# Kernel optimization log

Hardware: AMD Instinct MI355X
Metric: run time of the kernel (lower is better)

The kernel has to match this reference:

```python
import jax, jax.numpy as jnp
import numpy as np

B, H, S, DK = 2, 16, 2048, 64
NEG = -1000000000.0

def setup_inputs() -> dict:
    key = jax.random.key(0)
    k1, k2, k3, k4 = jax.random.split(key, 4)
    Q = jax.random.normal(k1, (B, H, S, DK), dtype=jnp.float32)
    K = jax.random.normal(k2, (B, H, S, DK), dtype=jnp.float32)
    V = jax.random.normal(k3, (B, H, S, DK), dtype=jnp.float32)
    mask = jax.random.randint(k4, (B, 1, S, S), 0, 2).astype(bool)
    return {"Q": Q, "K": K, "V": V, "mask": mask}

def reference(Q, K, V, mask):
    sqrt_dk = jnp.asarray(DK ** 0.5, Q.dtype)
    # [B,H,S,S] scores, materialized as in the original module
    score = jnp.einsum('bhqd,bhkd->bhqk', Q, K) / sqrt_dk
    score = jnp.where(mask, jnp.asarray(NEG, score.dtype), score)
    attn_prob = jax.nn.softmax(score, axis=-1)  # dropout p=0.0 -> identity
    context = jnp.einsum('bhqk,bhkd->bhqd', attn_prob, V)
    return (context, attn_prob)
```

## Files before the change

### kernel.cpp

```cpp
#include <hip/hip_runtime.h>

static constexpr int Bc  = 2;
static constexpr int Hc  = 16;
static constexpr int Sc  = 2048;
static constexpr int DKc = 64;
static constexpr float SC2  = 0.18033688011112043f;

typedef __attribute__((ext_vector_type(8)))  short short8v;
typedef __attribute__((ext_vector_type(16))) float f32x16;
typedef __attribute__((ext_vector_type(4)))  float f32x4;

__device__ __forceinline__ unsigned short f2bf(float f) {
    union { float f; unsigned u; } v; v.f = f;
    unsigned r = v.u + 0x7FFFu + ((v.u >> 16) & 1u);
    return (unsigned short)(r >> 16);
}
__device__ __forceinline__ unsigned cvtpk(float lo, float hi) {
    unsigned r;
    asm("v_cvt_pk_bf16_f32 %0, %1, %2" : "=v"(r) : "v"(lo), "v"(hi));
    return r;
}
__device__ __forceinline__ float fexp2(float x) {
    float r;
    asm("v_exp_f32 %0, %1" : "=v"(r) : "v"(x));
    return r;
}
__device__ __forceinline__ float bflo(unsigned u) {
    union { unsigned u; float f; } v; v.u = u << 16; return v.f;
}
__device__ __forceinline__ float bfhi(unsigned u) {
    union { unsigned u; float f; } v; v.u = u & 0xFFFF0000u; return v.f;
}

__global__ void kfrag_kernel(const float* __restrict__ K, unsigned short* __restrict__ Kf) {
    int i = blockIdx.x * 256 + threadIdx.x;
    int lane = i & 63, ks = (i >> 6) & 3, t = (i >> 8) & 63, bh = i >> 14;
    int hi = lane >> 5, l31 = lane & 31;
    const float* src = K + (((size_t)bh * Sc + t * 32 + l31) * DKc + ks * 16 + hi * 8);
    float4 a = *(const float4*)src;
    float4 c = *(const float4*)(src + 4);
    short8v s;
    s[0]=(short)f2bf(a.x); s[1]=(short)f2bf(a.y); s[2]=(short)f2bf(a.z); s[3]=(short)f2bf(a.w);
    s[4]=(short)f2bf(c.x); s[5]=(short)f2bf(c.y); s[6]=(short)f2bf(c.z); s[7]=(short)f2bf(c.w);
    *(short8v*)&Kf[(size_t)i * 8] = s;
}

__global__ void vfrag_kernel(const float* __restrict__ V, unsigned short* __restrict__ Vf) {
    int i = blockIdx.x * 256 + threadIdx.x;
    int lane = i & 63, dblk = (i >> 6) & 1, ks = (i >> 7) & 1, t = (i >> 8) & 63, bh = i >> 14;
    int hi = lane >> 5, l31 = lane & 31;
    int k0 = t * 32 + ks * 16 + hi * 8, d = dblk * 32 + l31;
    const float* vb = V + ((size_t)bh * Sc + k0) * DKc + d;
    short8v s;
    #pragma unroll
    for (int u = 0; u < 8; ++u) s[u] = (short)f2bf(vb[(size_t)u * DKc]);
    *(short8v*)&Vf[(size_t)i * 8] = s;
}

__global__ void mfrag_kernel(const int* __restrict__ M, unsigned* __restrict__ Mf) {
    int w = blockIdx.x * 4 + (threadIdx.x >> 6);
    int lane = threadIdx.x & 63;
    const int* row = M + (size_t)w * Sc;
    int b = w >> 11, q = w & 2047, qt = q >> 5, r = q & 31;
    unsigned* ob = Mf + (size_t)(b * 64 + qt) * 2048 + r;
    for (int tp = 0; tp < 32; ++tp) {
        unsigned long long bal = __ballot(row[tp * 64 + lane] != 0);
        if (lane == 0)  ob[(size_t)(2 * tp)     * 32] = (unsigned)bal;
        if (lane == 32) ob[(size_t)(2 * tp + 1) * 32] = (unsigned)(bal >> 32);
    }
}

__global__ __launch_bounds__(256, 2)
void attn_main(const float* __restrict__ Q, const unsigned short* __restrict__ Kf,
               const unsigned short* __restrict__ Vf, const unsigned* __restrict__ Mf,
               float* __restrict__ out)
{
    const int wg  = (int)blockIdx.x;
    const int swz = (wg & 7) * 256 + (wg >> 3);
    const int bh  = swz >> 6;
    const int qt  = swz & 63;
    const int qb  = qt << 5;
    const int b   = bh >> 4;

    const int tid  = (int)threadIdx.x;
    const int wid  = tid >> 6;
    const int lane = tid & 63;
    const int hi   = lane >> 5;
    const int l31  = lane & 31;

    __shared__ float lbuf[4][32];
    __shared__ float lfin[32];
    __shared__ char  sbuf[2][32768];

    const unsigned short* kfb = Kf + (size_t)bh * 131072;
    const unsigned short* vfb = Vf + (size_t)bh * 131072;
    const unsigned*       mfb = Mf + (size_t)(b * 64 + qt) * 2048;

    short8v qf[4];
    {
        const float* qrow = Q + ((size_t)bh * Sc + qb + l31) * DKc;
        #pragma unroll
        for (int ks = 0; ks < 4; ++ks) {
            const float* p0 = qrow + ks * 16 + hi * 8;
            float4 a = *(const float4*)p0;
            float4 c = *(const float4*)(p0 + 4);
            short8v f;
            f[0]=(short)f2bf(a.x); f[1]=(short)f2bf(a.y); f[2]=(short)f2bf(a.z); f[3]=(short)f2bf(a.w);
            f[4]=(short)f2bf(c.x); f[5]=(short)f2bf(c.y); f[6]=(short)f2bf(c.z); f[7]=(short)f2bf(c.w);
            qf[ks] = f;
        }
    }

    f32x16 acc0, acc1;
    #pragma unroll
    for (int u = 0; u < 16; ++u) { acc0[u] = 0.0f; acc1[u] = 0.0f; }

    unsigned ec[16][8];
    float l_run = 0.0f;

    #pragma unroll
    for (int i = 0; i < 16; ++i) {
        const int t = i * 4 + wid;
        short8v k4[4];
        #pragma unroll
        for (int ks = 0; ks < 4; ++ks)
            k4[ks] = *(const short8v*)&kfb[((size_t)(t * 4 + ks) * 64 + lane) * 8];
        short8v v4[4];
        #pragma unroll
        for (int u = 0; u < 4; ++u)
            v4[u] = *(const short8v*)&vfb[((size_t)(t * 4 + u) * 64 + lane) * 8];
        const unsigned mw = mfb[t * 32 + l31] >> (4 * hi);

        f32x16 sc;
        #pragma unroll
        for (int u = 0; u < 16; ++u) sc[u] = 0.0f;
        #pragma unroll
        for (int ks = 0; ks < 4; ++ks)
            sc = __builtin_amdgcn_mfma_f32_32x32x16_bf16(k4[ks], qf[ks], sc, 0, 0, 0);

        #pragma unroll
        for (int g = 0; g < 4; ++g)
            #pragma unroll
            for (int j = 0; j < 4; ++j) {
                float a = sc[4*g+j] * SC2;
                a = ((mw >> (8*g + j)) & 1u) ? -1e30f : a;
                sc[4*g+j] = fexp2(a);
            }

        float ps = 0.0f;
        #pragma unroll
        for (int u = 0; u < 16; ++u) ps += sc[u];
        ps += __shfl_xor(ps, 32);
        l_run += ps;

        #pragma unroll
        for (int g = 0; g < 4; ++g) {
            ec[i][2*g]   = cvtpk(sc[4*g],   sc[4*g+1]);
            ec[i][2*g+1] = cvtpk(sc[4*g+2], sc[4*g+3]);
        }

        #pragma unroll
        for (int ks = 0; ks < 2; ++ks) {
            unsigned o0x = ec[i][4*ks], o0y = ec[i][4*ks+1];
            unsigned o1x = ec[i][4*ks+2], o1y = ec[i][4*ks+3];
            unsigned s0x = __shfl_xor(o0x, 32), s0y = __shfl_xor(o0y, 32);
            unsigned s1x = __shfl_xor(o1x, 32), s1y = __shfl_xor(o1y, 32);
            union { unsigned u[4]; short8v s; } pa;
            pa.u[0] = hi ? s1x : o0x;
            pa.u[1] = hi ? s1y : o0y;
            pa.u[2] = hi ? o1x : s0x;
            pa.u[3] = hi ? o1y : s0y;
            acc0 = __builtin_amdgcn_mfma_f32_32x32x16_bf16(pa.s, v4[2*ks+0], acc0, 0, 0, 0);
            acc1 = __builtin_amdgcn_mfma_f32_32x32x16_bf16(pa.s, v4[2*ks+1], acc1, 0, 0, 0);
        }
    }

    if (hi == 0) lbuf[wid][l31] = l_run;
    __syncthreads();
    if (tid < 32) lfin[tid] = lbuf[0][tid] + lbuf[1][tid] + lbuf[2][tid] + lbuf[3][tid];
    __syncthreads();
    const float inv_l = 1.0f / lfin[l31];

    float* ctx   = out;
    float* attn  = out + (size_t)Bc * Hc * Sc * DKc;
    float* prow0 = attn + ((size_t)bh * Sc + qb) * Sc;

    #pragma unroll
    for (int r = 0; r < 8; ++r) {
        char* sb = &sbuf[r & 1][0];
        #pragma unroll
        for (int sub = 0; sub < 2; ++sub) {
            const int i = r * 2 + sub;
            #pragma unroll
            for (int g = 0; g < 4; ++g) {
                unsigned u0 = ec[i][2*g], u1 = ec[i][2*g+1];
                f32x4 st;
                st.x = bflo(u0) * inv_l; st.y = bfhi(u0) * inv_l;
                st.z = bflo(u1) * inv_l; st.w = bfhi(u1) * inv_l;
                *(f32x4*)(sb + sub * 16384 + l31 * 512 +
                          ((wid * 128 + 32*g + 16*hi) ^ ((l31 & 7) << 4))) = st;
            }
        }
        __syncthreads();
        #pragma unroll
        for (int j = 0; j < 8; ++j) {
            const int row = j * 4 + wid;
            f32x4 ld = *(const f32x4*)(&sbuf[r & 1][0] + (lane >> 5) * 16384 + row * 512 +
                                       (((lane & 31) * 16) ^ ((row & 7) << 4)));
            __builtin_nontemporal_store(ld, (f32x4*)(prow0 + (size_t)row * Sc + r * 256 + lane * 4));
        }
    }

    __syncthreads();
    float* pall = (float*)&sbuf[0][0];
    if (wid >= 2) {
        #pragma unroll
        for (int g = 0; g < 4; ++g)
            #pragma unroll
            for (int j = 0; j < 4; ++j) {
                int row = 8*g + 4*hi + j;
                pall[(wid - 2) * 2048 + row * 64 + l31]      = acc0[4*g+j];
                pall[(wid - 2) * 2048 + row * 64 + l31 + 32] = acc1[4*g+j];
            }
    }
    __syncthreads();
    if (wid < 2) {
        #pragma unroll
        for (int g = 0; g < 4; ++g)
            #pragma unroll
            for (int j = 0; j < 4; ++j) {
                int row = 8*g + 4*hi + j;
                acc0[4*g+j] += pall[wid * 2048 + row * 64 + l31];
                acc1[4*g+j] += pall[wid * 2048 + row * 64 + l31 + 32];
            }
    }
    __syncthreads();
    if (wid == 1) {
        #pragma unroll
        for (int g = 0; g < 4; ++g)
            #pragma unroll
            for (int j = 0; j < 4; ++j) {
                int row = 8*g + 4*hi + j;
                pall[row * 64 + l31]      = acc0[4*g+j];
                pall[row * 64 + l31 + 32] = acc1[4*g+j];
            }
    }
    __syncthreads();
    if (wid == 0) {
        #pragma unroll
        for (int g = 0; g < 4; ++g)
            #pragma unroll
            for (int j = 0; j < 4; ++j) {
                int row = 8*g + 4*hi + j;
                float rinv = 1.0f / lfin[row];
                float o0 = (acc0[4*g+j] + pall[row * 64 + l31])      * rinv;
                float o1 = (acc1[4*g+j] + pall[row * 64 + l31 + 32]) * rinv;
                size_t off = ((size_t)bh * Sc + qb + row) * DKc + l31;
                ctx[off]      = o0;
                ctx[off + 32] = o1;
            }
    }
}

extern "C" void kernel_launch(void* const* d_in, const int* in_sizes, int n_in,
                              void* d_out, int out_size, void* d_ws, size_t ws_size,
                              hipStream_t stream)
{
    const float* Q = (const float*)d_in[0];
    const float* K = (const float*)d_in[1];
    const float* V = (const float*)d_in[2];
    const int*   M = (const int*)d_in[3];
    float* out = (float*)d_out;

    unsigned short* Kf = (unsigned short*)d_ws;
    unsigned short* Vf = (unsigned short*)((char*)d_ws + (8u << 20));
    unsigned*       Mf = (unsigned*)((char*)d_ws + (16u << 20));

    hipLaunchKernelGGL(kfrag_kernel, dim3(2048), dim3(256), 0, stream, K, Kf);
    hipLaunchKernelGGL(vfrag_kernel, dim3(2048), dim3(256), 0, stream, V, Vf);
    hipLaunchKernelGGL(mfrag_kernel, dim3(1024), dim3(256), 0, stream, M, Mf);
    hipLaunchKernelGGL(attn_main,    dim3(2048), dim3(256), 0, stream, Q, Kf, Vf, Mf, out);
}
```

Measured before the change: 173.8 us.

## Make attention blocks persistent over four query tiles, overlapping prob stores with compute

Each workgroup now has 8 waves and loops over 4 consecutive query tiles of the same head instead of one. The attention-probability write-back for the previous tile is interleaved into the QK/PV loop of the next tile through a single shared staging buffer, so the heavy global store traffic overlaps with MFMA work. The split-K reduction across waves now has 8 partial accumulators. Costs include extra barriers inside the main loop, fewer workgroups (512), and more register pressure at 512 threads per block.

```diff
diff --git a/kernel.cpp b/kernel.cpp
--- a/kernel.cpp
+++ b/kernel.cpp
@@ -70,16 +70,15 @@
     }
 }
 
-__global__ __launch_bounds__(256, 2)
+__global__ __launch_bounds__(512, 2)
 void attn_main(const float* __restrict__ Q, const unsigned short* __restrict__ Kf,
                const unsigned short* __restrict__ Vf, const unsigned* __restrict__ Mf,
                float* __restrict__ out)
 {
     const int wg  = (int)blockIdx.x;
-    const int swz = (wg & 7) * 256 + (wg >> 3);
-    const int bh  = swz >> 6;
-    const int qt  = swz & 63;
-    const int qb  = qt << 5;
+    const int swz = (wg & 7) * 64 + (wg >> 3);
+    const int bh  = swz >> 4;
+    const int qt0 = (swz & 15) * 4;
     const int b   = bh >> 4;
 
     const int tid  = (int)threadIdx.x;
@@ -88,177 +87,237 @@
     const int hi   = lane >> 5;
     const int l31  = lane & 31;
 
-    __shared__ float lbuf[4][32];
+    __shared__ float lbuf[8][32];
     __shared__ float lfin[32];
-    __shared__ char  sbuf[2][32768];
+    __shared__ char  sbuf[32768];
 
     const unsigned short* kfb = Kf + (size_t)bh * 131072;
     const unsigned short* vfb = Vf + (size_t)bh * 131072;
-    const unsigned*       mfb = Mf + (size_t)(b * 64 + qt) * 2048;
-
-    short8v qf[4];
-    {
-        const float* qrow = Q + ((size_t)bh * Sc + qb + l31) * DKc;
+
+    float* ctx  = out;
+    float* attn = out + (size_t)Bc * Hc * Sc * DKc;
+
+    float  inv_prev  = 0.0f;
+    float* prow_prev = nullptr;
+
+    unsigned ec[8][8];
+
+    for (int tt = 0; tt < 4; ++tt) {
+        const int qt = qt0 + tt;
+        const int qb = qt * 32;
+        const unsigned* mfb = Mf + (size_t)(b * 64 + qt) * 2048;
+
+        short8v qf[4];
+        {
+            const float* qrow = Q + ((size_t)bh * Sc + qb + l31) * DKc;
+            #pragma unroll
+            for (int ks = 0; ks < 4; ++ks) {
+                const float* p0 = qrow + ks * 16 + hi * 8;
+                float4 a = *(const float4*)p0;
+                float4 c = *(const float4*)(p0 + 4);
+                short8v f;
+                f[0]=(short)f2bf(a.x); f[1]=(short)f2bf(a.y); f[2]=(short)f2bf(a.z); f[3]=(short)f2bf(a.w);
+                f[4]=(short)f2bf(c.x); f[5]=(short)f2bf(c.y); f[6]=(short)f2bf(c.z); f[7]=(short)f2bf(c.w);
+                qf[ks] = f;
+            }
+        }
+
+        f32x16 acc0, acc1;
         #pragma unroll
-        for (int ks = 0; ks < 4; ++ks) {
-            const float* p0 = qrow + ks * 16 + hi * 8;
-            float4 a = *(const float4*)p0;
-            float4 c = *(const float4*)(p0 + 4);
-            short8v f;
-            f[0]=(short)f2bf(a.x); f[1]=(short)f2bf(a.y); f[2]=(short)f2bf(a.z); f[3]=(short)f2bf(a.w);
-            f[4]=(short)f2bf(c.x); f[5]=(short)f2bf(c.y); f[6]=(short)f2bf(c.z); f[7]=(short)f2bf(c.w);
-            qf[ks] = f;
-        }
+        for (int u = 0; u < 16; ++u) { acc0[u] = 0.0f; acc1[u] = 0.0f; }
+        float l_run = 0.0f;
+
+        #pragma unroll
+        for (int i = 0; i < 8; ++i) {
+            if (tt > 0) {
+                __syncthreads();
+                #pragma unroll
+                for (int g = 0; g < 4; ++g) {
+                    unsigned u0 = ec[i][2*g], u1 = ec[i][2*g+1];
+                    f32x4 st;
+                    st.x = bflo(u0) * inv_prev; st.y = bfhi(u0) * inv_prev;
+                    st.z = bflo(u1) * inv_prev; st.w = bfhi(u1) * inv_prev;
+                    *(f32x4*)(sbuf + l31 * 1024 + wid * 128 +
+                              ((32*g + 16*hi) ^ ((l31 & 7) << 4))) = st;
+                }
+                __syncthreads();
+            }
+
+            const int t = i * 8 + wid;
+            short8v k4[4];
+            #pragma unroll
+            for (int ks = 0; ks < 4; ++ks)
+                k4[ks] = *(const short8v*)&kfb[((size_t)(t * 4 + ks) * 64 + lane) * 8];
+            short8v v4[4];
+            #pragma unroll
+            for (int u = 0; u < 4; ++u)
+                v4[u] = *(const short8v*)&vfb[((size_t)(t * 4 + u) * 64 + lane) * 8];
+            const unsigned mw = mfb[t * 32 + l31] >> (4 * hi);
+
+            if (tt > 0) {
+                #pragma unroll
+                for (int j = 0; j < 4; ++j) {
+                    const int row = j * 8 + wid;
+                    const int cb = lane * 16;
+                    f32x4 ld = *(const f32x4*)(sbuf + row * 1024 + (cb & ~127) +
+                                               ((cb & 127) ^ ((row & 7) << 4)));
+                    __builtin_nontemporal_store(ld,
+                        (f32x4*)(prow_prev + (size_t)row * Sc + i * 256 + lane * 4));
+                }
+            }
+
+            f32x16 sc;
+            #pragma unroll
+            for (int u = 0; u < 16; ++u) sc[u] = 0.0f;
+            #pragma unroll
+            for (int ks = 0; ks < 4; ++ks)
+                sc = __builtin_amdgcn_mfma_f32_32x32x16_bf16(k4[ks], qf[ks], sc, 0, 0, 0);
+
+            #pragma unroll
+            for (int g = 0; g < 4; ++g)
+                #pragma unroll
+                for (int j = 0; j < 4; ++j) {
+                    float a = sc[4*g+j] * SC2;
+                    a = ((mw >> (8*g + j)) & 1u) ? -1e30f : a;
+                    sc[4*g+j] = fexp2(a);
+                }
+
+            float ps = 0.0f;
+            #pragma unroll
+            for (int u = 0; u < 16; ++u) ps += sc[u];
+            ps += __shfl_xor(ps, 32);
+            l_run += ps;
+
+            #pragma unroll
+            for (int g = 0; g < 4; ++g) {
+                ec[i][2*g]   = cvtpk(sc[4*g],   sc[4*g+1]);
+                ec[i][2*g+1] = cvtpk(sc[4*g+2], sc[4*g+3]);
+            }
+
+            #pragma unroll
+            for (int ks = 0; ks < 2; ++ks) {
+                unsigned o0x = ec[i][4*ks], o0y = ec[i][4*ks+1];
+                unsigned o1x = ec[i][4*ks+2], o1y = ec[i][4*ks+3];
+                unsigned s0x = __shfl_xor(o0x, 32), s0y = __shfl_xor(o0y, 32);
+                unsigned s1x = __shfl_xor(o1x, 32), s1y = __shfl_xor(o1y, 32);
+                union { unsigned u[4]; short8v s; } pa;
+                pa.u[0] = hi ? s1x : o0x;
+                pa.u[1] = hi ? s1y : o0y;
+                pa.u[2] = hi ? o1x : s0x;
+                pa.u[3] = hi ? o1y : s0y;
+                acc0 = __builtin_amdgcn_mfma_f32_32x32x16_bf16(pa.s, v4[2*ks+0], acc0, 0, 0, 0);
+                acc1 = __builtin_amdgcn_mfma_f32_32x32x16_bf16(pa.s, v4[2*ks+1], acc1, 0, 0, 0);
+            }
+        }
+
+        if (hi == 0) lbuf[wid][l31] = l_run;
+        __syncthreads();
+        if (tid < 32) {
+            float l = 0.0f;
+            #pragma unroll
+            for (int w = 0; w < 8; ++w) l += lbuf[w][tid];
+            lfin[tid] = l;
+        }
+        __syncthreads();
+        const float invl = 1.0f / lfin[l31];
+
+        float* pall = (float*)sbuf;
+        if (wid >= 4) {
+            #pragma unroll
+            for (int g = 0; g < 4; ++g)
+                #pragma unroll
+                for (int j = 0; j < 4; ++j) {
+                    int row = 8*g + 4*hi + j;
+                    pall[(wid - 4) * 2048 + row * 64 + l31]      = acc0[4*g+j];
+                    pall[(wid - 4) * 2048 + row * 64 + l31 + 32] = acc1[4*g+j];
+                }
+        }
+        __syncthreads();
+        if (wid < 4) {
+            #pragma unroll
+            for (int g = 0; g < 4; ++g)
+                #pragma unroll
+                for (int j = 0; j < 4; ++j) {
+                    int row = 8*g + 4*hi + j;
+                    acc0[4*g+j] += pall[wid * 2048 + row * 64 + l31];
+                    acc1[4*g+j] += pall[wid * 2048 + row * 64 + l31 + 32];
+                }
+        }
+        __syncthreads();
+        if (wid == 2 || wid == 3) {
+            #pragma unroll
+            for (int g = 0; g < 4; ++g)
+                #pragma unroll
+                for (int j = 0; j < 4; ++j) {
+                    int row = 8*g + 4*hi + j;
+                    pall[(wid - 2) * 2048 + row * 64 + l31]      = acc0[4*g+j];
+                    pall[(wid - 2) * 2048 + row * 64 + l31 + 32] = acc1[4*g+j];
+                }
+        }
+        __syncthreads();
+        if (wid < 2) {
+            #pragma unroll
+            for (int g = 0; g < 4; ++g)
+                #pragma unroll
+                for (int j = 0; j < 4; ++j) {
+                    int row = 8*g + 4*hi + j;
+                    acc0[4*g+j] += pall[wid * 2048 + row * 64 + l31];
+                    acc1[4*g+j] += pall[wid * 2048 + row * 64 + l31 + 32];
+                }
+        }
+        __syncthreads();
+        if (wid == 1) {
+            #pragma unroll
+            for (int g = 0; g < 4; ++g)
+                #pragma unroll
+                for (int j = 0; j < 4; ++j) {
+                    int row = 8*g + 4*hi + j;
+                    pall[row * 64 + l31]      = acc0[4*g+j];
+                    pall[row * 64 + l31 + 32] = acc1[4*g+j];
+                }
+        }
+        __syncthreads();
+        if (wid == 0) {
+            #pragma unroll
+            for (int g = 0; g < 4; ++g)
+                #pragma unroll
+                for (int j = 0; j < 4; ++j) {
+                    int row = 8*g + 4*hi + j;
+                    float rinv = 1.0f / lfin[row];
+                    float o0 = (acc0[4*g+j] + pall[row * 64 + l31])      * rinv;
+                    float o1 = (acc1[4*g+j] + pall[row * 64 + l31 + 32]) * rinv;
+                    size_t off = ((size_t)bh * Sc + qb + row) * DKc + l31;
+                    ctx[off]      = o0;
+                    ctx[off + 32] = o1;
+                }
+        }
+
+        inv_prev  = invl;
+        prow_prev = attn + ((size_t)bh * Sc + qb) * Sc;
     }
 
-    f32x16 acc0, acc1;
     #pragma unroll
-    for (int u = 0; u < 16; ++u) { acc0[u] = 0.0f; acc1[u] = 0.0f; }
-
-    unsigned ec[16][8];
-    float l_run = 0.0f;
-
-    #pragma unroll
-    for (int i = 0; i < 16; ++i) {
-        const int t = i * 4 + wid;
-        short8v k4[4];
-        #pragma unroll
-        for (int ks = 0; ks < 4; ++ks)
-            k4[ks] = *(const short8v*)&kfb[((size_t)(t * 4 + ks) * 64 + lane) * 8];
-        short8v v4[4];
-        #pragma unroll
-        for (int u = 0; u < 4; ++u)
-            v4[u] = *(const short8v*)&vfb[((size_t)(t * 4 + u) * 64 + lane) * 8];
-        const unsigned mw = mfb[t * 32 + l31] >> (4 * hi);
-
-        f32x16 sc;
-        #pragma unroll
-        for (int u = 0; u < 16; ++u) sc[u] = 0.0f;
-        #pragma unroll
-        for (int ks = 0; ks < 4; ++ks)
-            sc = __builtin_amdgcn_mfma_f32_32x32x16_bf16(k4[ks], qf[ks], sc, 0, 0, 0);
-
-        #pragma unroll
-        for (int g = 0; g < 4; ++g)
-            #pragma unroll
-            for (int j = 0; j < 4; ++j) {
-                float a = sc[4*g+j] * SC2;
-                a = ((mw >> (8*g + j)) & 1u) ? -1e30f : a;
-                sc[4*g+j] = fexp2(a);
-            }
-
-        float ps = 0.0f;
-        #pragma unroll
-        for (int u = 0; u < 16; ++u) ps += sc[u];
-        ps += __shfl_xor(ps, 32);
-        l_run += ps;
-
+    for (int i = 0; i < 8; ++i) {
+        __syncthreads();
         #pragma unroll
         for (int g = 0; g < 4; ++g) {
-            ec[i][2*g]   = cvtpk(sc[4*g],   sc[4*g+1]);
-            ec[i][2*g+1] = cvtpk(sc[4*g+2], sc[4*g+3]);
-        }
-
+            unsigned u0 = ec[i][2*g], u1 = ec[i][2*g+1];
+            f32x4 st;
+            st.x = bflo(u0) * inv_prev; st.y = bfhi(u0) * inv_prev;
+            st.z = bflo(u1) * inv_prev; st.w = bfhi(u1) * inv_prev;
+            *(f32x4*)(sbuf + l31 * 1024 + wid * 128 +
+                      ((32*g + 16*hi) ^ ((l31 & 7) << 4))) = st;
+        }
+        __syncthreads();
         #pragma unroll
-        for (int ks = 0; ks < 2; ++ks) {
-            unsigned o0x = ec[i][4*ks], o0y = ec[i][4*ks+1];
-            unsigned o1x = ec[i][4*ks+2], o1y = ec[i][4*ks+3];
-            unsigned s0x = __shfl_xor(o0x, 32), s0y = __shfl_xor(o0y, 32);
-            unsigned s1x = __shfl_xor(o1x, 32), s1y = __shfl_xor(o1y, 32);
-            union { unsigned u[4]; short8v s; } pa;
-            pa.u[0] = hi ? s1x : o0x;
-            pa.u[1] = hi ? s1y : o0y;
-            pa.u[2] = hi ? o1x : s0x;
-            pa.u[3] = hi ? o1y : s0y;
-            acc0 = __builtin_amdgcn_mfma_f32_32x32x16_bf16(pa.s, v4[2*ks+0], acc0, 0, 0, 0);
-            acc1 = __builtin_amdgcn_mfma_f32_32x32x16_bf16(pa.s, v4[2*ks+1], acc1, 0, 0, 0);
-        }
-    }
-
-    if (hi == 0) lbuf[wid][l31] = l_run;
-    __syncthreads();
-    if (tid < 32) lfin[tid] = lbuf[0][tid] + lbuf[1][tid] + lbuf[2][tid] + lbuf[3][tid];
-    __syncthreads();
-    const float inv_l = 1.0f / lfin[l31];
-
-    float* ctx   = out;
-    float* attn  = out + (size_t)Bc * Hc * Sc * DKc;
-    float* prow0 = attn + ((size_t)bh * Sc + qb) * Sc;
-
-    #pragma unroll
-    for (int r = 0; r < 8; ++r) {
-        char* sb = &sbuf[r & 1][0];
-        #pragma unroll
-        for (int sub = 0; sub < 2; ++sub) {
-            const int i = r * 2 + sub;
-            #pragma unroll
-            for (int g = 0; g < 4; ++g) {
-                unsigned u0 = ec[i][2*g], u1 = ec[i][2*g+1];
-                f32x4 st;
-                st.x = bflo(u0) * inv_l; st.y = bfhi(u0) * inv_l;
-                st.z = bflo(u1) * inv_l; st.w = bfhi(u1) * inv_l;
-                *(f32x4*)(sb + sub * 16384 + l31 * 512 +
-                          ((wid * 128 + 32*g + 16*hi) ^ ((l31 & 7) << 4))) = st;
-            }
-        }
-        __syncthreads();
-        #pragma unroll
-        for (int j = 0; j < 8; ++j) {
-            const int row = j * 4 + wid;
-            f32x4 ld = *(const f32x4*)(&sbuf[r & 1][0] + (lane >> 5) * 16384 + row * 512 +
-                                       (((lane & 31) * 16) ^ ((row & 7) << 4)));
-            __builtin_nontemporal_store(ld, (f32x4*)(prow0 + (size_t)row * Sc + r * 256 + lane * 4));
-        }
-    }
-
-    __syncthreads();
-    float* pall = (float*)&sbuf[0][0];
-    if (wid >= 2) {
-        #pragma unroll
-        for (int g = 0; g < 4; ++g)
-            #pragma unroll
-            for (int j = 0; j < 4; ++j) {
-                int row = 8*g + 4*hi + j;
-                pall[(wid - 2) * 2048 + row * 64 + l31]      = acc0[4*g+j];
-                pall[(wid - 2) * 2048 + row * 64 + l31 + 32] = acc1[4*g+j];
-            }
-    }
-    __syncthreads();
-    if (wid < 2) {
-        #pragma unroll
-        for (int g = 0; g < 4; ++g)
-            #pragma unroll
-            for (int j = 0; j < 4; ++j) {
-                int row = 8*g + 4*hi + j;
-                acc0[4*g+j] += pall[wid * 2048 + row * 64 + l31];
-                acc1[4*g+j] += pall[wid * 2048 + row * 64 + l31 + 32];
-            }
-    }
-    __syncthreads();
-    if (wid == 1) {
-        #pragma unroll
-        for (int g = 0; g < 4; ++g)
-            #pragma unroll
-            for (int j = 0; j < 4; ++j) {
-                int row = 8*g + 4*hi + j;
-                pall[row * 64 + l31]      = acc0[4*g+j];
-                pall[row * 64 + l31 + 32] = acc1[4*g+j];
-            }
-    }
-    __syncthreads();
-    if (wid == 0) {
-        #pragma unroll
-        for (int g = 0; g < 4; ++g)
-            #pragma unroll
-            for (int j = 0; j < 4; ++j) {
-                int row = 8*g + 4*hi + j;
-                float rinv = 1.0f / lfin[row];
-                float o0 = (acc0[4*g+j] + pall[row * 64 + l31])      * rinv;
-                float o1 = (acc1[4*g+j] + pall[row * 64 + l31 + 32]) * rinv;
-                size_t off = ((size_t)bh * Sc + qb + row) * DKc + l31;
-                ctx[off]      = o0;
-                ctx[off + 32] = o1;
-            }
+        for (int j = 0; j < 4; ++j) {
+            const int row = j * 8 + wid;
+            const int cb = lane * 16;
+            f32x4 ld = *(const f32x4*)(sbuf + row * 1024 + (cb & ~127) +
+                                       ((cb & 127) ^ ((row & 7) << 4)));
+            __builtin_nontemporal_store(ld,
+                (f32x4*)(prow_prev + (size_t)row * Sc + i * 256 + lane * 4));
+        }
     }
 }
 
@@ -279,5 +338,5 @@
     hipLaunchKernelGGL(kfrag_kernel, dim3(2048), dim3(256), 0, stream, K, Kf);
     hipLaunchKernelGGL(vfrag_kernel, dim3(2048), dim3(256), 0, stream, V, Vf);
     hipLaunchKernelGGL(mfrag_kernel, dim3(1024), dim3(256), 0, stream, M, Mf);
-    hipLaunchKernelGGL(attn_main,    dim3(2048), dim3(256), 0, stream, Q, Kf, Vf, Mf, out);
-}
+    hipLaunchKernelGGL(attn_main,    dim3(512),  dim3(512), 0, stream, Q, Kf, Vf, Mf, out);
+}
```

After: 209.8 us. 20.7% more time.
